# Optimization experiments

Hardware: AMD Instinct MI355X
Metric: run time of the kernel (lower is better)

Reference implementation:

```python
import jax, jax.numpy as jnp
import numpy as np

N, E, G = 20000, 320000, 64   # nodes, edges, graphs in batch
DIN, DH, H, C = 128, 64, 8, 32  # in dim, hidden per head, heads, classes
NEG_SLOPE = 0.2


def setup_inputs() -> dict:
    key = jax.random.key(0)
    ks = jax.random.split(key, 20)
    s = lambda fan: 1.0 / np.sqrt(fan)
    inp = {
        "g_feats": jax.random.normal(ks[0], (N, DIN), jnp.float32),
        "src": jax.random.randint(ks[1], (E,), 0, N),
        "dst": jax.random.randint(ks[2], (E,), 0, N),
        "graph_ids": jnp.sort(jax.random.randint(ks[3], (N,), 0, G)),
        # input layer (linear): dim_in -> dim_h
        "W_in": jax.random.normal(ks[4], (DIN, DH), jnp.float32) * s(DIN),
        "b_in": jnp.zeros((DH,), jnp.float32),
        # GATv2 layer 1: dim_h -> H * dim_h
        "Wsrc1": jax.random.normal(ks[5], (DH, H * DH), jnp.float32) * s(DH),
        "bsrc1": jnp.zeros((H * DH,), jnp.float32),
        "Wdst1": jax.random.normal(ks[6], (DH, H * DH), jnp.float32) * s(DH),
        "bdst1": jnp.zeros((H * DH,), jnp.float32),
        "attn1": jax.random.normal(ks[7], (H, DH), jnp.float32) * s(DH),
        "bias1": jnp.zeros((H * DH,), jnp.float32),
        # GATv2 layer 2
        "Wsrc2": jax.random.normal(ks[8], (DH, H * DH), jnp.float32) * s(DH),
        "bsrc2": jnp.zeros((H * DH,), jnp.float32),
        "Wdst2": jax.random.normal(ks[9], (DH, H * DH), jnp.float32) * s(DH),
        "bdst2": jnp.zeros((H * DH,), jnp.float32),
        "attn2": jax.random.normal(ks[10], (H, DH), jnp.float32) * s(DH),
        "bias2": jnp.zeros((H * DH,), jnp.float32),
        # classification head: Linear(DH,DH) -> relu -> Linear(DH,C) -> softmax
        "Wh1": jax.random.normal(ks[11], (DH, DH), jnp.float32) * s(DH),
        "bh1": jnp.zeros((DH,), jnp.float32),
        "Wh2": jax.random.normal(ks[12], (DH, C), jnp.float32) * s(DH),
        "bh2": jnp.zeros((C,), jnp.float32),
    }
    return inp


def gatv2(h, src, dst, Ws, bs, Wd, bd, attn, bias):
    # DGL GATv2Conv: e_uv = attn . leaky_relu(fc_src(h_u) + fc_dst(h_v)),
    # softmax over incoming edges of v, aggregate fc_src(h_u).
    fs = (h @ Ws + bs).reshape(N, H, DH)
    fd = (h @ Wd + bd).reshape(N, H, DH)
    e = jax.nn.leaky_relu(fs[src] + fd[dst], NEG_SLOPE)      # [E, H, DH]
    scores = jnp.einsum('ehd,hd->eh', e, attn)               # [E, H]
    m = jax.ops.segment_max(scores, dst, num_segments=N)     # [N, H]
    m = jnp.where(jnp.isfinite(m), m, 0.0)                   # nodes w/o in-edges
    w = jnp.exp(scores - m[dst])
    denom = jax.ops.segment_sum(w, dst, num_segments=N)
    alpha = w / jnp.maximum(denom[dst], 1e-9)                # [E, H]
    out = jax.ops.segment_sum(fs[src] * alpha[:, :, None], dst, num_segments=N)
    return out + bias.reshape(1, H, DH)                      # [N, H, DH]


def reference(g_feats, src, dst, graph_ids, W_in, b_in,
              Wsrc1, bsrc1, Wdst1, bdst1, attn1, bias1,
              Wsrc2, bsrc2, Wdst2, bdst2, attn2, bias2,
              Wh1, bh1, Wh2, bh2):
    h = g_feats @ W_in + b_in                                # input layer ('linear')
    h = gatv2(h, src, dst, Wsrc1, bsrc1, Wdst1, bdst1, attn1, bias1).mean(axis=1)
    h = jax.nn.relu(h)
    h = gatv2(h, src, dst, Wsrc2, bsrc2, Wdst2, bdst2, attn2, bias2).mean(axis=1)
    # mean readout per graph
    sums = jax.ops.segment_sum(h, graph_ids, num_segments=G)
    counts = jax.ops.segment_sum(jnp.ones((N,), h.dtype), graph_ids, num_segments=G)
    hg = sums / jnp.maximum(counts, 1.0)[:, None]            # [G, DH]
    # head: Linear -> relu -> Linear -> softmax (dropout = identity at eval)
    logits = jax.nn.relu(hg @ Wh1 + bh1) @ Wh2 + bh2
    return jax.nn.softmax(logits, axis=-1)
```

## Files before the change

### kernel.cpp

```cpp
#include <hip/hip_runtime.h>

#define NN 20000
#define NE 320000
#define NG 64
#define DIN 128
#define DH 64
#define NH 8
#define HD 512
#define NC 32

typedef unsigned short ushort_t;
typedef unsigned int uint_t;

__device__ __forceinline__ ushort_t f2bf(float f) {
  uint_t x = __float_as_uint(f);
  uint_t r = (x + 0x7fffu + ((x >> 16) & 1u)) >> 16;
  return (ushort_t)r;
}

template<int PAT>
__device__ __forceinline__ float swz(float v) {
  return __int_as_float(__builtin_amdgcn_ds_swizzle(__float_as_int(v), PAT));
}

__device__ __forceinline__ void gemm_in_tile(const float* __restrict__ gf,
    const float* __restrict__ W_in, const float* __restrict__ b_in,
    float* __restrict__ h0, int tile) {
  __shared__ float AsIn[16][DIN];
  const int t = threadIdx.x;
  const int row0 = tile * 16;
  for (int i = t; i < 16 * DIN; i += 256)
    AsIn[i >> 7][i & 127] = gf[(size_t)(row0 + (i >> 7)) * DIN + (i & 127)];
  __syncthreads();
  const int c = t & 63, rg = t >> 6;
  float acc[4] = {0.f, 0.f, 0.f, 0.f};
  for (int k = 0; k < DIN; ++k) {
    float w = W_in[k * DH + c];
#pragma unroll
    for (int i = 0; i < 4; ++i) acc[i] += AsIn[rg * 4 + i][k] * w;
  }
  float b = b_in[c];
#pragma unroll
  for (int i = 0; i < 4; ++i)
    h0[(size_t)(row0 + rg * 4 + i) * DH + c] = acc[i] + b;
}

__device__ __forceinline__ void pair_tile(const float* __restrict__ A,
    const float* __restrict__ Ws, const float* __restrict__ bs,
    const float* __restrict__ Wd, const float* __restrict__ bd,
    ushort_t* __restrict__ fsb, float* __restrict__ fd, int tile) {
  __shared__ float AsP[16][DH];
  const int t = threadIdx.x;
  const bool isFd = tile >= (NN / 16);
  const int bx = isFd ? tile - (NN / 16) : tile;
  const float* W = isFd ? Wd : Ws;
  const float* b = isFd ? bd : bs;
  const int row0 = bx * 16;
  {
    int idx = t * 4;
    int r = idx >> 6, k = idx & 63;
    *(float4*)&AsP[r][k] = *(const float4*)&A[(size_t)(row0 + r) * DH + k];
  }
  __syncthreads();
  const int tc = t & 127;
  const int tr = t >> 7;
  float acc[8][4];
#pragma unroll
  for (int r = 0; r < 8; ++r)
#pragma unroll
    for (int c = 0; c < 4; ++c) acc[r][c] = 0.f;
#pragma unroll 4
  for (int k = 0; k < DH; ++k) {
    float4 wv = *(const float4*)&W[k * HD + 4 * tc];
#pragma unroll
    for (int r = 0; r < 8; ++r) {
      float a = AsP[tr * 8 + r][k];
      acc[r][0] += a * wv.x; acc[r][1] += a * wv.y;
      acc[r][2] += a * wv.z; acc[r][3] += a * wv.w;
    }
  }
  float4 bv = *(const float4*)&b[4 * tc];
#pragma unroll
  for (int r = 0; r < 8; ++r) {
    int row = row0 + tr * 8 + r;
    float v0 = acc[r][0] + bv.x, v1 = acc[r][1] + bv.y;
    float v2 = acc[r][2] + bv.z, v3 = acc[r][3] + bv.w;
    if (!isFd) {
      ushort4 o;
      o.x = f2bf(v0); o.y = f2bf(v1); o.z = f2bf(v2); o.w = f2bf(v3);
      *(ushort4*)&fsb[(size_t)row * HD + 4 * tc] = o;
    } else {
      *(float4*)&fd[(size_t)row * HD + 4 * tc] = make_float4(v0, v1, v2, v3);
    }
  }
}

__global__ __launch_bounds__(256) void k_pre(const float* __restrict__ gf,
    const float* __restrict__ W_in, const float* __restrict__ b_in,
    float* __restrict__ h0, const int* __restrict__ dst, int* __restrict__ counts,
    const int* __restrict__ gid, int* __restrict__ gs) {
  const int bid = blockIdx.x;
  if (bid < NN / 16) {
    gemm_in_tile(gf, W_in, b_in, h0, bid);
  } else if (bid < NN / 16 + NE / 256) {
    int e = (bid - NN / 16) * 256 + threadIdx.x;
    atomicAdd(&counts[dst[e]], 1);
  } else {
    int i = (bid - (NN / 16 + NE / 256)) * 256 + threadIdx.x;
    if (i > NN) return;
    if (i == 0) {
      for (int g = 0; g <= gid[0]; ++g) gs[g] = 0;
    } else if (i == NN) {
      for (int g = gid[NN - 1] + 1; g <= NG; ++g) gs[g] = NN;
    } else {
      int a = gid[i - 1], b2 = gid[i];
      for (int g = a + 1; g <= b2; ++g) gs[g] = i;
    }
  }
}

__global__ __launch_bounds__(256) void k_scan(const int* __restrict__ counts,
    int* __restrict__ row_start, int* __restrict__ cursor) {
  __shared__ int ps[256];
  const int t = threadIdx.x;
  const int CH = (NN + 255) / 256;
  int base = t * CH;
  int s = 0;
  for (int i = 0; i < CH; ++i) {
    int idx = base + i;
    if (idx < NN) s += counts[idx];
  }
  ps[t] = s;
  __syncthreads();
  for (int off = 1; off < 256; off <<= 1) {
    int v = (t >= off) ? ps[t - off] : 0;
    __syncthreads();
    ps[t] += v;
    __syncthreads();
  }
  int prefix = (t > 0) ? ps[t - 1] : 0;
  for (int i = 0; i < CH; ++i) {
    int idx = base + i;
    if (idx < NN) {
      row_start[idx] = prefix;
      cursor[idx] = prefix;
      prefix += counts[idx];
    }
  }
  if (t == 255) row_start[NN] = ps[255];
}

__global__ __launch_bounds__(256) void k_scatpair(const float* __restrict__ A,
    const float* __restrict__ Ws, const float* __restrict__ bs,
    const float* __restrict__ Wd, const float* __restrict__ bd,
    ushort_t* __restrict__ fsb, float* __restrict__ fd,
    const int* __restrict__ dst, const int* __restrict__ src,
    int* __restrict__ cursor, int* __restrict__ src_sorted) {
  const int bid = blockIdx.x;
  if (bid < 2 * (NN / 16)) {
    pair_tile(A, Ws, bs, Wd, bd, fsb, fd, bid);
  } else {
    int e = (bid - 2 * (NN / 16)) * 256 + threadIdx.x;
    int p = atomicAdd(&cursor[dst[e]], 1);
    src_sorted[p] = src[e];
  }
}

__global__ __launch_bounds__(256) void k_pair(const float* __restrict__ A,
    const float* __restrict__ Ws, const float* __restrict__ bs,
    const float* __restrict__ Wd, const float* __restrict__ bd,
    ushort_t* __restrict__ fsb, float* __restrict__ fd) {
  pair_tile(A, Ws, bs, Wd, bd, fsb, fd, blockIdx.x);
}

__global__ __launch_bounds__(256) void k_gat(const ushort_t* __restrict__ fsb,
    const float* __restrict__ fd, const int* __restrict__ src_sorted,
    const int* __restrict__ row_start, const float* __restrict__ attn,
    const float* __restrict__ bias, float* __restrict__ hout, int do_relu) {
  const int lane = threadIdx.x & 63;
  const int v = blockIdx.x * 4 + (threadIdx.x >> 6);
  const int fi = lane * 8;
  float fdv[8], av[8];
  *(float4*)&fdv[0] = *(const float4*)&fd[(size_t)v * HD + fi];
  *(float4*)&fdv[4] = *(const float4*)&fd[(size_t)v * HD + fi + 4];
  *(float4*)&av[0]  = *(const float4*)&attn[fi];
  *(float4*)&av[4]  = *(const float4*)&attn[fi + 4];
  int e = row_start[v];
  const int end = row_start[v + 1];
  float m = -3.4e38f, sum = 0.f;
  float acc[8];
#pragma unroll
  for (int i = 0; i < 8; ++i) acc[i] = 0.f;
  for (; e + 1 < end; e += 2) {
    int sA = src_sorted[e], sB = src_sorted[e + 1];
    uint4 uA = *(const uint4*)&fsb[(size_t)sA * HD + fi];
    uint4 uB = *(const uint4*)&fsb[(size_t)sB * HD + fi];
    float fA[8], fB[8];
    fA[0] = __uint_as_float(uA.x << 16); fA[1] = __uint_as_float(uA.x & 0xffff0000u);
    fA[2] = __uint_as_float(uA.y << 16); fA[3] = __uint_as_float(uA.y & 0xffff0000u);
    fA[4] = __uint_as_float(uA.z << 16); fA[5] = __uint_as_float(uA.z & 0xffff0000u);
    fA[6] = __uint_as_float(uA.w << 16); fA[7] = __uint_as_float(uA.w & 0xffff0000u);
    fB[0] = __uint_as_float(uB.x << 16); fB[1] = __uint_as_float(uB.x & 0xffff0000u);
    fB[2] = __uint_as_float(uB.y << 16); fB[3] = __uint_as_float(uB.y & 0xffff0000u);
    fB[4] = __uint_as_float(uB.z << 16); fB[5] = __uint_as_float(uB.z & 0xffff0000u);
    fB[6] = __uint_as_float(uB.w << 16); fB[7] = __uint_as_float(uB.w & 0xffff0000u);
    float pA = 0.f, pB = 0.f;
#pragma unroll
    for (int i = 0; i < 8; ++i) {
      float xA = fA[i] + fdv[i];
      float lA = fmaxf(xA, 0.f) + 0.2f * fminf(xA, 0.f);
      pA = fmaf(av[i], lA, pA);
      float xB = fB[i] + fdv[i];
      float lB = fmaxf(xB, 0.f) + 0.2f * fminf(xB, 0.f);
      pB = fmaf(av[i], lB, pB);
    }
    pA += swz<0x041F>(pA); pB += swz<0x041F>(pB);
    pA += swz<0x081F>(pA); pB += swz<0x081F>(pB);
    pA += swz<0x101F>(pA); pB += swz<0x101F>(pB);
    float mn = fmaxf(m, fmaxf(pA, pB));
    float scale = __expf(m - mn);
    float wA = __expf(pA - mn), wB = __expf(pB - mn);
    sum = fmaf(sum, scale, wA + wB);
#pragma unroll
    for (int i = 0; i < 8; ++i)
      acc[i] = fmaf(acc[i], scale, fmaf(wA, fA[i], wB * fB[i]));
    m = mn;
  }
  if (e < end) {
    int sA = src_sorted[e];
    uint4 uA = *(const uint4*)&fsb[(size_t)sA * HD + fi];
    float fA[8];
    fA[0] = __uint_as_float(uA.x << 16); fA[1] = __uint_as_float(uA.x & 0xffff0000u);
    fA[2] = __uint_as_float(uA.y << 16); fA[3] = __uint_as_float(uA.y & 0xffff0000u);
    fA[4] = __uint_as_float(uA.z << 16); fA[5] = __uint_as_float(uA.z & 0xffff0000u);
    fA[6] = __uint_as_float(uA.w << 16); fA[7] = __uint_as_float(uA.w & 0xffff0000u);
    float pA = 0.f;
#pragma unroll
    for (int i = 0; i < 8; ++i) {
      float xA = fA[i] + fdv[i];
      float lA = fmaxf(xA, 0.f) + 0.2f * fminf(xA, 0.f);
      pA = fmaf(av[i], lA, pA);
    }
    pA += swz<0x041F>(pA);
    pA += swz<0x081F>(pA);
    pA += swz<0x101F>(pA);
    float mn = fmaxf(m, pA);
    float scale = __expf(m - mn);
    float wA = __expf(pA - mn);
    sum = fmaf(sum, scale, wA);
#pragma unroll
    for (int i = 0; i < 8; ++i)
      acc[i] = fmaf(acc[i], scale, wA * fA[i]);
  }
  float inv = 1.f / fmaxf(sum, 1e-9f);
  float outv[8];
#pragma unroll
  for (int i = 0; i < 8; ++i) outv[i] = fmaf(acc[i], inv, bias[fi + i]);
#pragma unroll
  for (int i = 0; i < 8; ++i) {
    outv[i] += swz<0x201F>(outv[i]);
    outv[i] += swz<0x401F>(outv[i]);
    outv[i] += __shfl_xor(outv[i], 32);
    outv[i] *= 0.125f;
    if (do_relu) outv[i] = fmaxf(outv[i], 0.f);
  }
  if (lane < 8) {
    *(float4*)&hout[(size_t)v * DH + lane * 8]     = make_float4(outv[0], outv[1], outv[2], outv[3]);
    *(float4*)&hout[(size_t)v * DH + lane * 8 + 4] = make_float4(outv[4], outv[5], outv[6], outv[7]);
  }
}

__global__ __launch_bounds__(256) void k_head(const float* __restrict__ h2,
    const int* __restrict__ gsv, const float* __restrict__ Wh1,
    const float* __restrict__ bh1, const float* __restrict__ Wh2,
    const float* __restrict__ bh2, float* __restrict__ out) {
  __shared__ float part[4][DH];
  __shared__ float hg[DH];
  __shared__ float hid[DH];
  __shared__ float logits[NC];
  const int g = blockIdx.x;
  const int t = threadIdx.x;
  const int f = t & 63, chunk = t >> 6;
  int start = gsv[g], stop = gsv[g + 1];
  float s = 0.f;
  for (int r = start + chunk; r < stop; r += 4) s += h2[(size_t)r * DH + f];
  part[chunk][f] = s;
  __syncthreads();
  if (t < DH) {
    float tot = part[0][t] + part[1][t] + part[2][t] + part[3][t];
    hg[t] = tot / fmaxf((float)(stop - start), 1.f);
  }
  __syncthreads();
  if (t < DH) {
    float a = 0.f;
    for (int k = 0; k < DH; ++k) a += hg[k] * Wh1[k * DH + t];
    hid[t] = fmaxf(a + bh1[t], 0.f);
  }
  __syncthreads();
  if (t < NC) {
    float l = 0.f;
    for (int k = 0; k < DH; ++k) l += hid[k] * Wh2[k * NC + t];
    logits[t] = l + bh2[t];
  }
  __syncthreads();
  if (t == 0) {
    float mx = logits[0];
    for (int i = 1; i < NC; ++i) mx = fmaxf(mx, logits[i]);
    float sm = 0.f;
    for (int i = 0; i < NC; ++i) {
      float wv = __expf(logits[i] - mx);
      logits[i] = wv;
      sm += wv;
    }
    float inv = 1.f / sm;
    for (int i = 0; i < NC; ++i) out[g * NC + i] = logits[i] * inv;
  }
}

extern "C" void kernel_launch(void* const* d_in, const int* in_sizes, int n_in,
                              void* d_out, int out_size, void* d_ws, size_t ws_size,
                              hipStream_t stream) {
  const float* g_feats = (const float*)d_in[0];
  const int*   src     = (const int*)d_in[1];
  const int*   dst     = (const int*)d_in[2];
  const int*   gid     = (const int*)d_in[3];
  const float* W_in    = (const float*)d_in[4];
  const float* b_in    = (const float*)d_in[5];
  const float* Wsrc1   = (const float*)d_in[6];
  const float* bsrc1   = (const float*)d_in[7];
  const float* Wdst1   = (const float*)d_in[8];
  const float* bdst1   = (const float*)d_in[9];
  const float* attn1   = (const float*)d_in[10];
  const float* bias1   = (const float*)d_in[11];
  const float* Wsrc2   = (const float*)d_in[12];
  const float* bsrc2   = (const float*)d_in[13];
  const float* Wdst2   = (const float*)d_in[14];
  const float* bdst2   = (const float*)d_in[15];
  const float* attn2   = (const float*)d_in[16];
  const float* bias2   = (const float*)d_in[17];
  const float* Wh1     = (const float*)d_in[18];
  const float* bh1     = (const float*)d_in[19];
  const float* Wh2     = (const float*)d_in[20];
  const float* bh2     = (const float*)d_in[21];

  char* ws = (char*)d_ws;
  size_t off = 0;
  auto A = [&](size_t bytes) -> char* {
    char* q = ws + off;
    off = (off + bytes + 255) & ~(size_t)255;
    return q;
  };
  float*    h0         = (float*)A((size_t)NN * DH * 4);
  float*    h1         = (float*)A((size_t)NN * DH * 4);
  float*    h2         = (float*)A((size_t)NN * DH * 4);
  ushort_t* fsb        = (ushort_t*)A((size_t)NN * HD * 2);
  float*    fd         = (float*)A((size_t)NN * HD * 4);
  int*      row_start  = (int*)A((size_t)(NN + 1) * 4);
  int*      cursor     = (int*)A((size_t)NN * 4);
  int*      src_sorted = (int*)A((size_t)NE * 4);
  int*      gs         = (int*)A((size_t)(NG + 1) * 4);
  int*      counts     = (int*)A((size_t)NN * 4);

  const int nb16 = NN / 16;
  const int histb = NE / 256;
  const int gbb = (NN + 256) / 256;

  hipMemsetAsync(counts, 0, (size_t)NN * 4, stream);

  k_pre<<<nb16 + histb + gbb, 256, 0, stream>>>(g_feats, W_in, b_in, h0,
                                                dst, counts, gid, gs);
  k_scan<<<1, 256, 0, stream>>>(counts, row_start, cursor);
  k_scatpair<<<2 * nb16 + histb, 256, 0, stream>>>(h0, Wsrc1, bsrc1, Wdst1, bdst1,
                                                   fsb, fd, dst, src, cursor, src_sorted);
  k_gat<<<NN / 4, 256, 0, stream>>>(fsb, fd, src_sorted, row_start, attn1, bias1, h1, 1);
  k_pair<<<2 * nb16, 256, 0, stream>>>(h1, Wsrc2, bsrc2, Wdst2, bdst2, fsb, fd);
  k_gat<<<NN / 4, 256, 0, stream>>>(fsb, fd, src_sorted, row_start, attn2, bias2, h2, 0);
  k_head<<<NG, 256, 0, stream>>>(h2, gs, Wh1, bh1, Wh2, bh2, (float*)d_out);
}
```

Baseline: 399.0 us.

## Replace single-block prefix scan with atomic per-wavefront segment allocation

Replaces the single-block serial exclusive scan over node in-degree counts with a many-block kernel. Each wavefront does a shuffle-based local scan and claims its slice of the edge array with one atomicAdd on a global counter. Segments are therefore no longer in node order, so the CSR offsets become separate begin and end arrays consumed by the GAT kernels. This removes the latency of a one-block scan, at the cost of non-deterministic segment placement that may reduce locality of src_sorted reads for neighbouring nodes.

```diff
diff --git a/kernel.cpp b/kernel.cpp
--- a/kernel.cpp
+++ b/kernel.cpp
@@ -119,35 +119,29 @@
   }
 }
 
-__global__ __launch_bounds__(256) void k_scan(const int* __restrict__ counts,
-    int* __restrict__ row_start, int* __restrict__ cursor) {
-  __shared__ int ps[256];
-  const int t = threadIdx.x;
-  const int CH = (NN + 255) / 256;
-  int base = t * CH;
-  int s = 0;
-  for (int i = 0; i < CH; ++i) {
-    int idx = base + i;
-    if (idx < NN) s += counts[idx];
-  }
-  ps[t] = s;
-  __syncthreads();
-  for (int off = 1; off < 256; off <<= 1) {
-    int v = (t >= off) ? ps[t - off] : 0;
-    __syncthreads();
-    ps[t] += v;
-    __syncthreads();
-  }
-  int prefix = (t > 0) ? ps[t - 1] : 0;
-  for (int i = 0; i < CH; ++i) {
-    int idx = base + i;
-    if (idx < NN) {
-      row_start[idx] = prefix;
-      cursor[idx] = prefix;
-      prefix += counts[idx];
-    }
-  }
-  if (t == 255) row_start[NN] = ps[255];
+__global__ __launch_bounds__(256) void k_assign(const int* __restrict__ counts,
+    int* __restrict__ row_beg, int* __restrict__ row_end, int* __restrict__ cursor,
+    int* __restrict__ gcounter) {
+  const int i = blockIdx.x * 256 + threadIdx.x;
+  const int lane = threadIdx.x & 63;
+  int cnt = (i < NN) ? counts[i] : 0;
+  int pre = cnt;
+#pragma unroll
+  for (int d = 1; d < 64; d <<= 1) {
+    int o = __shfl_up(pre, d);
+    if (lane >= d) pre += o;
+  }
+  int total = __shfl(pre, 63);
+  int excl = pre - cnt;
+  int base = 0;
+  if (lane == 63 && total > 0) base = atomicAdd(gcounter, total);
+  base = __shfl(base, 63);
+  if (i < NN) {
+    int b = base + excl;
+    row_beg[i] = b;
+    row_end[i] = b + cnt;
+    cursor[i] = b;
+  }
 }
 
 __global__ __launch_bounds__(256) void k_scatpair(const float* __restrict__ A,
@@ -175,8 +169,9 @@
 
 __global__ __launch_bounds__(256) void k_gat(const ushort_t* __restrict__ fsb,
     const float* __restrict__ fd, const int* __restrict__ src_sorted,
-    const int* __restrict__ row_start, const float* __restrict__ attn,
-    const float* __restrict__ bias, float* __restrict__ hout, int do_relu) {
+    const int* __restrict__ row_beg, const int* __restrict__ row_end,
+    const float* __restrict__ attn, const float* __restrict__ bias,
+    float* __restrict__ hout, int do_relu) {
   const int lane = threadIdx.x & 63;
   const int v = blockIdx.x * 4 + (threadIdx.x >> 6);
   const int fi = lane * 8;
@@ -185,8 +180,8 @@
   *(float4*)&fdv[4] = *(const float4*)&fd[(size_t)v * HD + fi + 4];
   *(float4*)&av[0]  = *(const float4*)&attn[fi];
   *(float4*)&av[4]  = *(const float4*)&attn[fi + 4];
-  int e = row_start[v];
-  const int end = row_start[v + 1];
+  int e = row_beg[v];
+  const int end = row_end[v];
   float m = -3.4e38f, sum = 0.f;
   float acc[8];
 #pragma unroll
@@ -355,25 +350,29 @@
   float*    h2         = (float*)A((size_t)NN * DH * 4);
   ushort_t* fsb        = (ushort_t*)A((size_t)NN * HD * 2);
   float*    fd         = (float*)A((size_t)NN * HD * 4);
-  int*      row_start  = (int*)A((size_t)(NN + 1) * 4);
+  int*      row_beg    = (int*)A((size_t)NN * 4);
+  int*      row_end    = (int*)A((size_t)NN * 4);
   int*      cursor     = (int*)A((size_t)NN * 4);
   int*      src_sorted = (int*)A((size_t)NE * 4);
   int*      gs         = (int*)A((size_t)(NG + 1) * 4);
-  int*      counts     = (int*)A((size_t)NN * 4);
+  int*      counts     = (int*)A((size_t)(NN + 1) * 4);
 
   const int nb16 = NN / 16;
   const int histb = NE / 256;
   const int gbb = (NN + 256) / 256;
 
-  hipMemsetAsync(counts, 0, (size_t)NN * 4, stream);
+  hipMemsetAsync(counts, 0, (size_t)(NN + 1) * 4, stream);
 
   k_pre<<<nb16 + histb + gbb, 256, 0, stream>>>(g_feats, W_in, b_in, h0,
                                                 dst, counts, gid, gs);
-  k_scan<<<1, 256, 0, stream>>>(counts, row_start, cursor);
+  k_assign<<<(NN + 255) / 256, 256, 0, stream>>>(counts, row_beg, row_end,
+                                                 cursor, &counts[NN]);
   k_scatpair<<<2 * nb16 + histb, 256, 0, stream>>>(h0, Wsrc1, bsrc1, Wdst1, bdst1,
                                                    fsb, fd, dst, src, cursor, src_sorted);
-  k_gat<<<NN / 4, 256, 0, stream>>>(fsb, fd, src_sorted, row_start, attn1, bias1, h1, 1);
+  k_gat<<<NN / 4, 256, 0, stream>>>(fsb, fd, src_sorted, row_beg, row_end,
+                                    attn1, bias1, h1, 1);
   k_pair<<<2 * nb16, 256, 0, stream>>>(h1, Wsrc2, bsrc2, Wdst2, bdst2, fsb, fd);
-  k_gat<<<NN / 4, 256, 0, stream>>>(fsb, fd, src_sorted, row_start, attn2, bias2, h2, 0);
+  k_gat<<<NN / 4, 256, 0, stream>>>(fsb, fd, src_sorted, row_beg, row_end,
+                                    attn2, bias2, h2, 0);
   k_head<<<NG, 256, 0, stream>>>(h2, gs, Wh1, bh1, Wh2, bh2, (float*)d_out);
 }
```

New measurement: 341.8 us. 1.17x faster.
